# Kernel optimization log

Measured on AMD Instinct MI355X. Metric: run time of the kernel, lower is better.

The kernel has to match this reference:

```python
import jax, jax.numpy as jnp
import numpy as np

B, N_IN, N_OUT = 16, 512, 4096
IN_CH, OUT_CH = 1, 64
HIDDEN = 2 * IN_CH  # normalize=True -> density channel + value channels
INIT_LENGTH_SCALE = 0.1


def setup_inputs() -> dict:
    key = jax.random.key(0)
    k1, k2, k3, k4, k5 = jax.random.split(key, 5)
    x = jax.random.uniform(k1, (B, N_IN, 1), dtype=jnp.float32)
    y = jax.random.normal(k2, (B, N_IN, IN_CH), dtype=jnp.float32)
    t = jax.random.uniform(k3, (B, N_OUT, 1), dtype=jnp.float32)
    # learned params
    sigma = jnp.full((HIDDEN,), np.log(INIT_LENGTH_SCALE), dtype=jnp.float32)
    # xavier_normal for fc.weight (out, in)
    std = float(np.sqrt(2.0 / (HIDDEN + OUT_CH)))
    W = jax.random.normal(k4, (OUT_CH, HIDDEN), dtype=jnp.float32) * std
    b = jnp.zeros((OUT_CH,), dtype=jnp.float32)
    return {"x": x, "y": y, "t": t, "sigma": sigma, "W": W, "b": b}


def reference(x, y, t, sigma, W, b):
    eps = 1e-8
    # compute_dists: (B, n_in, n_out) squared distances (1-D inputs)
    dists = (x - jnp.transpose(t, (0, 2, 1))) ** 2  # (B, n_in, n_out)
    scales = jnp.exp(sigma)  # (hidden,)
    # rbf weights: (B, n_in, n_out, hidden)
    wt = jnp.exp(-0.5 * dists[..., None] / scales ** 2)
    # normalize=True: prepend density channel of ones
    density = jnp.ones((x.shape[0], x.shape[1], IN_CH), dtype=y.dtype)
    y_out = jnp.concatenate([density, y], axis=2)  # (B, n_in, hidden)
    # weighted neighbor aggregation: sum over n_in
    agg = jnp.einsum('bnc,bnmc->bmc', y_out, wt)  # (B, n_out, hidden)
    dens, conv = agg[..., :IN_CH], agg[..., IN_CH:]
    normalized = conv / (dens + eps)
    feats = jnp.concatenate([dens, normalized], axis=-1)  # (B, n_out, hidden)
    # BatchLinear: plain linear over last dim
    out = jnp.einsum('bmc,oc->bmo', feats, W) + b  # (B, n_out, out_ch)
    return out
```

## Files before the change

kernel.cpp:

```cpp
#include <hip/hip_runtime.h>
#include <hip/hip_bf16.h>

#define NB 16
#define N_IN 512
#define N_OUT 4096
#define OUT_CH 64
#define M_TILE 64
#define NCHUNK 4
#define NPER (N_IN / NCHUNK)

__global__ __launch_bounds__(256) void convdeepset_kernel(
    const float* __restrict__ x,
    const float* __restrict__ y,
    const float* __restrict__ t,
    const float* __restrict__ sigma,
    const float* __restrict__ W,
    const float* __restrict__ bias,
    float* __restrict__ out)
{
    __shared__ float xs[N_IN];
    __shared__ float ys[N_IN];
    __shared__ float red0[256];
    __shared__ float red1[256];
    __shared__ float f0[M_TILE];
    __shared__ float f1[M_TILE];
    __shared__ float wf[OUT_CH * 2];
    __shared__ float bf[OUT_CH];

    const int tid = threadIdx.x;
    const int blk = blockIdx.x;
    const int b   = blk >> 6;
    const int mt  = blk & 63;
    const int m0  = mt * M_TILE;

    for (int i = tid; i < N_IN; i += 256) {
        xs[i] = x[b * N_IN + i];
        ys[i] = y[b * N_IN + i];
    }
    if (tid < OUT_CH * 2) wf[tid] = W[tid];
    if (tid < OUT_CH)     bf[tid] = bias[tid];
    __syncthreads();

    const int ml = tid & 63;
    const int nc = tid >> 6;
    const int m  = m0 + ml;
    const float tm = t[b * N_OUT + m];

    const float LOG2E = 1.4426950408889634f;
    const float s0 = sigma[0];
    const float s1 = sigma[1];
    const float k0 = -0.5f * __builtin_amdgcn_exp2f(-2.0f * s0 * LOG2E) * LOG2E;
    const float k1 = -0.5f * __builtin_amdgcn_exp2f(-2.0f * s1 * LOG2E) * LOG2E;

    float a0 = 0.0f, a1 = 0.0f;
    const int nbase = nc * NPER;

    if (k0 == k1) {
        #pragma unroll 8
        for (int i = 0; i < NPER; ++i) {
            float dx = xs[nbase + i] - tm;
            float e  = __builtin_amdgcn_exp2f(k0 * dx * dx);
            a0 += e;
            a1 = fmaf(ys[nbase + i], e, a1);
        }
    } else {
        #pragma unroll 8
        for (int i = 0; i < NPER; ++i) {
            float dx = xs[nbase + i] - tm;
            float d2 = dx * dx;
            a0 += __builtin_amdgcn_exp2f(k0 * d2);
            a1 = fmaf(ys[nbase + i], __builtin_amdgcn_exp2f(k1 * d2), a1);
        }
    }

    red0[tid] = a0;
    red1[tid] = a1;
    __syncthreads();

    if (tid < M_TILE) {
        float dens = red0[tid] + red0[tid + 64] + red0[tid + 128] + red0[tid + 192];
        float conv = red1[tid] + red1[tid + 64] + red1[tid + 128] + red1[tid + 192];
        f0[tid] = dens;
        f1[tid] = conv / (dens + 1e-8f);
    }
    __syncthreads();

    const size_t obase = (size_t)(b * N_OUT + m0) * OUT_CH;
    for (int p = tid; p < M_TILE * OUT_CH / 4; p += 256) {
        int mloc = p >> 4;
        int o    = (p & 15) * 4;
        float d = f0[mloc], nrm = f1[mloc];
        float4 v;
        v.x = fmaf(wf[2 * (o + 0) + 0], d, fmaf(wf[2 * (o + 0) + 1], nrm, bf[o + 0]));
        v.y = fmaf(wf[2 * (o + 1) + 0], d, fmaf(wf[2 * (o + 1) + 1], nrm, bf[o + 1]));
        v.z = fmaf(wf[2 * (o + 2) + 0], d, fmaf(wf[2 * (o + 2) + 1], nrm, bf[o + 2]));
        v.w = fmaf(wf[2 * (o + 3) + 0], d, fmaf(wf[2 * (o + 3) + 1], nrm, bf[o + 3]));
        *reinterpret_cast<float4*>(out + obase + (size_t)mloc * OUT_CH + o) = v;
    }
}

extern "C" void kernel_launch(void* const* d_in, const int* in_sizes, int n_in,
                              void* d_out, int out_size, void* d_ws, size_t ws_size,
                              hipStream_t stream) {
    const float* x     = (const float*)d_in[0];
    const float* y     = (const float*)d_in[1];
    const float* t     = (const float*)d_in[2];
    const float* sigma = (const float*)d_in[3];
    const float* W     = (const float*)d_in[4];
    const float* bias  = (const float*)d_in[5];
    float* out = (float*)d_out;

    dim3 grid(NB * (N_OUT / M_TILE));
    convdeepset_kernel<<<grid, 256, 0, stream>>>(x, y, t, sigma, W, bias, out);
}
```

Baseline: 75.75 us.

## Expand squared distance algebraically and compute two outputs per thread

When both length scales are equal, the squared-distance exponent is expanded as k·x² − 2k·x·t + k·t². The per-input terms are precomputed once into a packed float4 in shared memory, so the inner loop needs only one FMA plus the exp2. The exp2(k·t²) factor is pulled out of the sum and applied once at the end. Each thread now handles two output points (M_TILE 128), which spreads each shared-memory load across two evaluations but halves the number of blocks. The expanded form can produce large intermediate exponents before rescaling, which risks precision loss and fewer waves in flight.

```diff
diff --git a/kernel.cpp b/kernel.cpp
--- a/kernel.cpp
+++ b/kernel.cpp
@@ -5,7 +5,7 @@
 #define N_IN 512
 #define N_OUT 4096
 #define OUT_CH 64
-#define M_TILE 64
+#define M_TILE 128
 #define NCHUNK 4
 #define NPER (N_IN / NCHUNK)
 
@@ -18,10 +18,9 @@
     const float* __restrict__ bias,
     float* __restrict__ out)
 {
-    __shared__ float xs[N_IN];
-    __shared__ float ys[N_IN];
-    __shared__ float red0[256];
-    __shared__ float red1[256];
+    __shared__ float4 pqyx[N_IN];
+    __shared__ float red0[2][256];
+    __shared__ float red1[2][256];
     __shared__ float f0[M_TILE];
     __shared__ float f1[M_TILE];
     __shared__ float wf[OUT_CH * 2];
@@ -29,57 +28,77 @@
 
     const int tid = threadIdx.x;
     const int blk = blockIdx.x;
-    const int b   = blk >> 6;
-    const int mt  = blk & 63;
+    const int b   = blk >> 5;
+    const int mt  = blk & 31;
     const int m0  = mt * M_TILE;
-
-    for (int i = tid; i < N_IN; i += 256) {
-        xs[i] = x[b * N_IN + i];
-        ys[i] = y[b * N_IN + i];
-    }
-    if (tid < OUT_CH * 2) wf[tid] = W[tid];
-    if (tid < OUT_CH)     bf[tid] = bias[tid];
-    __syncthreads();
-
-    const int ml = tid & 63;
-    const int nc = tid >> 6;
-    const int m  = m0 + ml;
-    const float tm = t[b * N_OUT + m];
 
     const float LOG2E = 1.4426950408889634f;
     const float s0 = sigma[0];
     const float s1 = sigma[1];
     const float k0 = -0.5f * __builtin_amdgcn_exp2f(-2.0f * s0 * LOG2E) * LOG2E;
     const float k1 = -0.5f * __builtin_amdgcn_exp2f(-2.0f * s1 * LOG2E) * LOG2E;
+    const bool fast = (k0 == k1);
 
-    float a0 = 0.0f, a1 = 0.0f;
+    for (int i = tid; i < N_IN; i += 256) {
+        float xv = x[b * N_IN + i];
+        float yv = y[b * N_IN + i];
+        float4 f;
+        f.x = k0 * xv * xv;
+        f.y = -2.0f * k0 * xv;
+        f.z = yv;
+        f.w = xv;
+        pqyx[i] = f;
+    }
+    if (tid < OUT_CH * 2) wf[tid] = W[tid];
+    if (tid < OUT_CH)     bf[tid] = bias[tid];
+    __syncthreads();
+
+    const int l  = tid & 63;
+    const int nc = tid >> 6;
     const int nbase = nc * NPER;
 
-    if (k0 == k1) {
-        #pragma unroll 8
+    const float t0 = t[b * N_OUT + m0 + l];
+    const float t1 = t[b * N_OUT + m0 + 64 + l];
+
+    float a00 = 0.0f, a01 = 0.0f;
+    float a10 = 0.0f, a11 = 0.0f;
+
+    if (fast) {
+        #pragma unroll 4
         for (int i = 0; i < NPER; ++i) {
-            float dx = xs[nbase + i] - tm;
-            float e  = __builtin_amdgcn_exp2f(k0 * dx * dx);
-            a0 += e;
-            a1 = fmaf(ys[nbase + i], e, a1);
+            float4 f = pqyx[nbase + i];
+            float e0 = __builtin_amdgcn_exp2f(fmaf(f.y, t0, f.x));
+            float e1 = __builtin_amdgcn_exp2f(fmaf(f.y, t1, f.x));
+            a00 += e0;
+            a01 = fmaf(f.z, e0, a01);
+            a10 += e1;
+            a11 = fmaf(f.z, e1, a11);
         }
+        const float et0 = __builtin_amdgcn_exp2f(k0 * t0 * t0);
+        const float et1 = __builtin_amdgcn_exp2f(k0 * t1 * t1);
+        a00 *= et0; a01 *= et0;
+        a10 *= et1; a11 *= et1;
     } else {
-        #pragma unroll 8
+        #pragma unroll 4
         for (int i = 0; i < NPER; ++i) {
-            float dx = xs[nbase + i] - tm;
-            float d2 = dx * dx;
-            a0 += __builtin_amdgcn_exp2f(k0 * d2);
-            a1 = fmaf(ys[nbase + i], __builtin_amdgcn_exp2f(k1 * d2), a1);
+            float4 f = pqyx[nbase + i];
+            float dx0 = f.w - t0, dx1 = f.w - t1;
+            float d20 = dx0 * dx0, d21 = dx1 * dx1;
+            a00 += __builtin_amdgcn_exp2f(k0 * d20);
+            a01 = fmaf(f.z, __builtin_amdgcn_exp2f(k1 * d20), a01);
+            a10 += __builtin_amdgcn_exp2f(k0 * d21);
+            a11 = fmaf(f.z, __builtin_amdgcn_exp2f(k1 * d21), a11);
         }
     }
 
-    red0[tid] = a0;
-    red1[tid] = a1;
+    red0[0][tid] = a00; red1[0][tid] = a01;
+    red0[1][tid] = a10; red1[1][tid] = a11;
     __syncthreads();
 
     if (tid < M_TILE) {
-        float dens = red0[tid] + red0[tid + 64] + red0[tid + 128] + red0[tid + 192];
-        float conv = red1[tid] + red1[tid + 64] + red1[tid + 128] + red1[tid + 192];
+        const int h = tid >> 6, ll = tid & 63;
+        float dens = red0[h][ll] + red0[h][ll + 64] + red0[h][ll + 128] + red0[h][ll + 192];
+        float conv = red1[h][ll] + red1[h][ll + 64] + red1[h][ll + 128] + red1[h][ll + 192];
         f0[tid] = dens;
         f1[tid] = conv / (dens + 1e-8f);
     }
```

Result: no change. 76.53 us (+1.0%).
